# Kernel tuning notes

Hardware: AMD Instinct MI355X
Metric: run time of the kernel (lower is better)

## Reference

```python
import jax, jax.numpy as jnp
import numpy as np

H = 128        # hidden_dim
NP = 512       # program nodes
NV = 50000     # voxel nodes
E = 800000     # cross edges (16 per voxel)
TAU = 1.0
SLOPE = 0.01   # LeakyReLU default negative slope


def setup_inputs() -> dict:
    key = jax.random.key(0)
    ks = jax.random.split(key, 12)
    s = 1.0 / np.sqrt(H)
    x = jax.random.normal(ks[0], (NP, H), dtype=jnp.float32)
    v = jax.random.normal(ks[1], (NV, H), dtype=jnp.float32)
    row0 = jax.random.randint(ks[2], (E,), 0, NP, dtype=jnp.int32)
    row1 = (jnp.arange(E, dtype=jnp.int32) % NV)  # every voxel gets E/NV edges
    cross_edge_index = jnp.stack([row0, row1])    # [2, E]
    W_program = jax.random.normal(ks[3], (H, H), dtype=jnp.float32) * s
    b_program = jnp.zeros((H,), dtype=jnp.float32)
    W_voxel = jax.random.normal(ks[4], (H, H), dtype=jnp.float32) * s
    b_voxel = jnp.zeros((H,), dtype=jnp.float32)
    W_m1 = jax.random.normal(ks[5], (H, H), dtype=jnp.float32) * s
    b_m1 = jnp.zeros((H,), dtype=jnp.float32)
    W_m2 = jax.random.normal(ks[6], (H, 1), dtype=jnp.float32) * s
    b_m2 = jnp.zeros((1,), dtype=jnp.float32)
    theta = jax.random.normal(ks[7], (H, 1), dtype=jnp.float32) * s  # xavier-like
    u = jax.random.uniform(ks[8], (E,), dtype=jnp.float32)
    gumbel_u = jnp.clip(u, 1e-7, 1.0 - 1e-7)  # avoid log(0)
    return {"x": x, "v": v, "cross_edge_index": cross_edge_index,
            "W_program": W_program, "b_program": b_program,
            "W_voxel": W_voxel, "b_voxel": b_voxel,
            "W_m1": W_m1, "b_m1": b_m1, "W_m2": W_m2, "b_m2": b_m2,
            "theta": theta, "gumbel_u": gumbel_u}


def reference(x, v, cross_edge_index, W_program, b_program, W_voxel, b_voxel,
              W_m1, b_m1, W_m2, b_m2, theta, gumbel_u):
    src = cross_edge_index[0]
    dst = cross_edge_index[1]
    x_sel = x[src]                      # [E, H] gather
    v_sel = v[dst]                      # [E, H] gather
    # mask = sigmoid(MLP(v)) : Linear -> LeakyReLU -> Linear(H,1)
    a = v @ W_m1 + b_m1
    a = jnp.where(a >= 0, a, SLOPE * a)
    mask = jax.nn.sigmoid(a @ W_m2 + b_m2)                  # [NV, 1]
    # attention logits: theta^T * tanh(Wp x_sel + Wv v_sel), summed over H
    t = jnp.tanh(x_sel @ W_program + b_program + v_sel @ W_voxel + b_voxel)
    e = jnp.sum(t * theta[:, 0], axis=-1)                   # [E]
    # Gumbel softmax: global softmax over all edges (dim=0 in torch on 1-D e)
    g = -jnp.log(-jnp.log(gumbel_u))
    y = jax.nn.softmax((e + g) / TAU)                       # [E]
    # per-voxel hard argmax (scatter_max), straight-through estimator
    seg_max = jax.ops.segment_max(y, dst, num_segments=NV)  # [NV]
    is_max = y == seg_max[dst]
    cand = jnp.where(is_max, jnp.arange(E), E)
    argmax = jax.ops.segment_min(cand, dst, num_segments=NV)  # [NV], first max per voxel
    y_hard_1 = jnp.zeros(E + 1, y.dtype).at[argmax].set(1.0)[:E]  # overflow slot for empty segments
    y_hard = jax.lax.stop_gradient(y_hard_1 - y) + y
    # scatter-sum of soft-attended program features back to voxels
    summed = jax.ops.segment_sum(x_sel * y[:, None], dst, num_segments=NV)  # [NV, H]
    v_out = v + mask * summed
    return (v_out, mask, y[:, None], y_hard[:, None])
```

## Files before the change

kernel.cpp:

```cpp
#include <hip/hip_runtime.h>

#define H     128
#define NP    512
#define NVOX  50000
#define NEDGE 800000
#define EPV   16
#define SLOPE 0.01f
#define GR    16
#define NBLK  (NVOX / GR)
#define STRH  136
#define VSTR  132
#define C1    2.8853900817779268f
#define LOG2E 1.4426950408889634f
#define ABLK  3125

#define EXP2(x) __builtin_amdgcn_exp2f(x)
#define LOG2(x) __builtin_amdgcn_logf(x)
#define RCP(x)  __builtin_amdgcn_rcpf(x)

typedef _Float16 h16;
typedef __attribute__((ext_vector_type(4))) _Float16 h16x4;
typedef __attribute__((ext_vector_type(8))) _Float16 h16x8;
typedef __attribute__((ext_vector_type(4))) float    f32x4;

__global__ __launch_bounds__(256) void k_pre(const float* __restrict__ x,
                                             const float* __restrict__ Wp,
                                             const float* __restrict__ bp,
                                             const float* __restrict__ Wv,
                                             const float* __restrict__ Wm1,
                                             float* __restrict__ xpout,
                                             h16* __restrict__ WvThi,
                                             h16* __restrict__ WvTlo,
                                             h16* __restrict__ Wm1T) {
    __shared__ float part[H];
    int bid = blockIdx.x;
    int tid = threadIdx.x;
    if (bid < NP) {
        int row = bid;
        int col = tid & 127;
        int kh  = tid >> 7;
        int kbase = kh * 64;
        const float* xr = x + (size_t)row * H;
        float acc = 0.f;
#pragma unroll 8
        for (int k = 0; k < 64; ++k)
            acc = fmaf(xr[kbase + k], Wp[(size_t)(kbase + k) * H + col], acc);
        if (kh == 1) part[col] = acc;
        __syncthreads();
        if (kh == 0) xpout[(size_t)row * H + col] = (acc + part[col] + bp[col]) * C1;
    } else {
        int idx = (bid - NP) * 256 + tid;
        if (idx < 16384) {
            int k = idx >> 7, n = idx & 127;
            float w = Wv[idx];
            h16 hi = (h16)w;
            WvThi[n * H + k] = hi;
            WvTlo[n * H + k] = (h16)(w - (float)hi);
        } else {
            int j = idx - 16384;
            int k = j >> 7, n = j & 127;
            Wm1T[n * H + k] = (h16)Wm1[j];
        }
    }
}

__global__ __launch_bounds__(256) void k_main(
    const float* __restrict__ v,   const float* __restrict__ x,
    const float* __restrict__ bv,  const float* __restrict__ bm1,
    const float* __restrict__ Wm2, const float* __restrict__ bm2,
    const h16* __restrict__ WvThi, const h16* __restrict__ WvTlo,
    const h16* __restrict__ Wm1T,
    const float* __restrict__ xp,  const int* __restrict__ cei,
    const float* __restrict__ theta, const float* __restrict__ gum,
    float* __restrict__ mask_out, float* __restrict__ pout,
    float* __restrict__ sump,     float* __restrict__ partial)
{
    __shared__ __align__(16) char ldsbuf[2 * GR * STRH * 2];
    h16*   vh   = (h16*)ldsbuf;
    h16*   vl   = vh + GR * STRH;
    float* vt   = (float*)ldsbuf;
    float* scmb = (float*)ldsbuf;
    __shared__ float ptile[EPV * GR];
    __shared__ int   ceit[EPV * GR];
    __shared__ float gumt[EPV * GR];
    __shared__ int   amtile[GR];
    __shared__ float pmbuf[4][GR];
    __shared__ float psums[4];

    int tid  = threadIdx.x;
    int base = blockIdx.x * GR;

#pragma unroll
    for (int i = 0; i < 2; ++i) {
        int f  = i * 256 + tid;
        int r  = f >> 5, c4 = f & 31;
        float4 val = *(const float4*)&v[(size_t)(base + r) * H + c4 * 4];
        h16x4 hi, lo;
        hi.x = (h16)val.x; lo.x = (h16)(val.x - (float)hi.x);
        hi.y = (h16)val.y; lo.y = (h16)(val.y - (float)hi.y);
        hi.z = (h16)val.z; lo.z = (h16)(val.z - (float)hi.z);
        hi.w = (h16)val.w; lo.w = (h16)(val.w - (float)hi.w);
        *(h16x4*)&vh[r * STRH + c4 * 4] = hi;
        *(h16x4*)&vl[r * STRH + c4 * 4] = lo;
    }
    {
        int t = tid >> 4, c = tid & 15;
        int e = base + c + t * NVOX;
        ceit[tid] = cei[e];
        gumt[tid] = gum[e];
    }
    __syncthreads();

    int wave = tid >> 6, lane = tid & 63;
    int m16 = lane & 15, quad = lane >> 4;
    int cb = wave * 32;

    f32x4 aV[2], aM[2];
#pragma unroll
    for (int ct = 0; ct < 2; ++ct) { aV[ct] = (f32x4)0.f; aM[ct] = (f32x4)0.f; }

#pragma unroll
    for (int kc = 0; kc < 4; ++kc) {
        int kofs = kc * 32 + quad * 8;
        h16x8 ah = *(const h16x8*)&vh[m16 * STRH + kofs];
        h16x8 al = *(const h16x8*)&vl[m16 * STRH + kofs];
#pragma unroll
        for (int ct = 0; ct < 2; ++ct) {
            int n = cb + ct * 16 + m16;
            h16x8 bh = *(const h16x8*)&WvThi[n * H + kofs];
            h16x8 bl = *(const h16x8*)&WvTlo[n * H + kofs];
            h16x8 bm = *(const h16x8*)&Wm1T[n * H + kofs];
            aV[ct] = __builtin_amdgcn_mfma_f32_16x16x32_f16(ah, bh, aV[ct], 0, 0, 0);
            aV[ct] = __builtin_amdgcn_mfma_f32_16x16x32_f16(al, bh, aV[ct], 0, 0, 0);
            aV[ct] = __builtin_amdgcn_mfma_f32_16x16x32_f16(ah, bl, aV[ct], 0, 0, 0);
            aM[ct] = __builtin_amdgcn_mfma_f32_16x16x32_f16(ah, bm, aM[ct], 0, 0, 0);
        }
    }
    __syncthreads();

    float pml[4] = {0.f, 0.f, 0.f, 0.f};
#pragma unroll
    for (int ct = 0; ct < 2; ++ct) {
        int col = cb + ct * 16 + m16;
        float bvc = bv[col], bmc = bm1[col], w2c = Wm2[col];
#pragma unroll
        for (int reg = 0; reg < 4; ++reg) {
            int row = quad * 4 + reg;
            vt[row * VSTR + col] = (aV[ct][reg] + bvc) * C1;
            float m = aM[ct][reg] + bmc;
            m = (m >= 0.f) ? m : SLOPE * m;
            pml[reg] = fmaf(m, w2c, pml[reg]);
        }
    }
#pragma unroll
    for (int off = 8; off >= 1; off >>= 1)
#pragma unroll
        for (int reg = 0; reg < 4; ++reg)
            pml[reg] += __shfl_xor(pml[reg], off, 64);
    if (m16 == 0) {
#pragma unroll
        for (int reg = 0; reg < 4; ++reg)
            pmbuf[wave][quad * 4 + reg] = pml[reg];
    }
    __syncthreads();
    if (wave == 0 && lane < GR) {
        float s = pmbuf[0][lane] + pmbuf[1][lane] + pmbuf[2][lane]
                + pmbuf[3][lane] + bm2[0];
        mask_out[base + lane] = RCP(1.f + EXP2(-s * LOG2E));
    }

    int g = tid >> 3, lk = tid & 7;
    int vx = g & 15, half = g >> 4;
    float th2[16], thsum = 0.f;
#pragma unroll
    for (int i = 0; i < 4; ++i) {
        float4 t4 = *(const float4*)&theta[(lk + 8 * i) * 4];
        th2[i * 4 + 0] = -2.f * LOG2E * t4.x; th2[i * 4 + 1] = -2.f * LOG2E * t4.y;
        th2[i * 4 + 2] = -2.f * LOG2E * t4.z; th2[i * 4 + 3] = -2.f * LOG2E * t4.w;
        thsum += LOG2E * (t4.x + t4.y + t4.z + t4.w);
    }
    const float* vr = &vt[vx * VSTR];
    float4 b0 = *(const float4*)&vr[(lk +  0) * 4];
    float4 b1 = *(const float4*)&vr[(lk +  8) * 4];
    float4 b2 = *(const float4*)&vr[(lk + 16) * 4];
    float4 b3 = *(const float4*)&vr[(lk + 24) * 4];
    float wv8[8];
#pragma unroll
    for (int i = 0; i < 8; ++i)
        wv8[i] = -LOG2E * RCP(LOG2(gumt[(half * 8 + i) * GR + vx]));
    __syncthreads();

    float4 s0 = make_float4(0.f,0.f,0.f,0.f), s1 = s0, s2 = s0, s3 = s0;
#pragma unroll 2
    for (int i = 0; i < 8; ++i) {
        int t   = half * 8 + i;
        int src = ceit[t * GR + vx];
        const float4* xr = (const float4*)(xp + (size_t)src * H);
        const float4* xo = (const float4*)(x  + (size_t)src * H);
        float4 a0 = xr[lk], a1 = xr[lk + 8], a2 = xr[lk + 16], a3 = xr[lk + 24];
        float4 c0 = xo[lk], c1 = xo[lk + 8], c2 = xo[lk + 16], c3 = xo[lk + 24];
        float acc0 = thsum, acc1 = 0.f;
        acc0 = fmaf(th2[ 0], RCP(EXP2(a0.x + b0.x) + 1.f), acc0);
        acc1 = fmaf(th2[ 1], RCP(EXP2(a0.y + b0.y) + 1.f), acc1);
        acc0 = fmaf(th2[ 2], RCP(EXP2(a0.z + b0.z) + 1.f), acc0);
        acc1 = fmaf(th2[ 3], RCP(EXP2(a0.w + b0.w) + 1.f), acc1);
        acc0 = fmaf(th2[ 4], RCP(EXP2(a1.x + b1.x) + 1.f), acc0);
        acc1 = fmaf(th2[ 5], RCP(EXP2(a1.y + b1.y) + 1.f), acc1);
        acc0 = fmaf(th2[ 6], RCP(EXP2(a1.z + b1.z) + 1.f), acc0);
        acc1 = fmaf(th2[ 7], RCP(EXP2(a1.w + b1.w) + 1.f), acc1);
        acc0 = fmaf(th2[ 8], RCP(EXP2(a2.x + b2.x) + 1.f), acc0);
        acc1 = fmaf(th2[ 9], RCP(EXP2(a2.y + b2.y) + 1.f), acc1);
        acc0 = fmaf(th2[10], RCP(EXP2(a2.z + b2.z) + 1.f), acc0);
        acc1 = fmaf(th2[11], RCP(EXP2(a2.w + b2.w) + 1.f), acc1);
        acc0 = fmaf(th2[12], RCP(EXP2(a3.x + b3.x) + 1.f), acc0);
        acc1 = fmaf(th2[13], RCP(EXP2(a3.y + b3.y) + 1.f), acc1);
        acc0 = fmaf(th2[14], RCP(EXP2(a3.z + b3.z) + 1.f), acc0);
        acc1 = fmaf(th2[15], RCP(EXP2(a3.w + b3.w) + 1.f), acc1);
        float acc = acc0 + acc1;
        acc += __shfl_xor(acc, 4, 64);
        acc += __shfl_xor(acc, 2, 64);
        acc += __shfl_xor(acc, 1, 64);
        float p = EXP2(acc) * wv8[i];
        if (lk == 0) ptile[t * GR + vx] = p;
        s0.x = fmaf(p, c0.x, s0.x); s0.y = fmaf(p, c0.y, s0.y);
        s0.z = fmaf(p, c0.z, s0.z); s0.w = fmaf(p, c0.w, s0.w);
        s1.x = fmaf(p, c1.x, s1.x); s1.y = fmaf(p, c1.y, s1.y);
        s1.z = fmaf(p, c1.z, s1.z); s1.w = fmaf(p, c1.w, s1.w);
        s2.x = fmaf(p, c2.x, s2.x); s2.y = fmaf(p, c2.y, s2.y);
        s2.z = fmaf(p, c2.z, s2.z); s2.w = fmaf(p, c2.w, s2.w);
        s3.x = fmaf(p, c3.x, s3.x); s3.y = fmaf(p, c3.y, s3.y);
        s3.z = fmaf(p, c3.z, s3.z); s3.w = fmaf(p, c3.w, s3.w);
    }
    if (half == 1) {
        float* sc = scmb + vx * 128;
        *(float4*)&sc[(lk +  0) * 4] = s0;
        *(float4*)&sc[(lk +  8) * 4] = s1;
        *(float4*)&sc[(lk + 16) * 4] = s2;
        *(float4*)&sc[(lk + 24) * 4] = s3;
    }
    __syncthreads();
    if (tid < GR) {
        float mx = ptile[tid]; int a = 0;
#pragma unroll
        for (int t = 1; t < EPV; ++t) {
            float yv = ptile[t * GR + tid];
            if (yv > mx) { mx = yv; a = t; }
        }
        amtile[tid] = a;
    }
    if (half == 0) {
        const float* sc = scmb + vx * 128;
        float4 r0 = *(const float4*)&sc[(lk +  0) * 4];
        float4 r1 = *(const float4*)&sc[(lk +  8) * 4];
        float4 r2 = *(const float4*)&sc[(lk + 16) * 4];
        float4 r3 = *(const float4*)&sc[(lk + 24) * 4];
        float* sr = sump + (size_t)(base + vx) * H;
        *(float4*)&sr[(lk +  0) * 4] = make_float4(s0.x+r0.x, s0.y+r0.y, s0.z+r0.z, s0.w+r0.w);
        *(float4*)&sr[(lk +  8) * 4] = make_float4(s1.x+r1.x, s1.y+r1.y, s1.z+r1.z, s1.w+r1.w);
        *(float4*)&sr[(lk + 16) * 4] = make_float4(s2.x+r2.x, s2.y+r2.y, s2.z+r2.z, s2.w+r2.w);
        *(float4*)&sr[(lk + 24) * 4] = make_float4(s3.x+r3.x, s3.y+r3.y, s3.z+r3.z, s3.w+r3.w);
    }
    __syncthreads();
    float pv;
    {
        int t = tid >> 4, c = tid & 15;
        pv = ptile[tid];
        pout[base + c + t * NVOX] = (t == amtile[c]) ? -pv : pv;
    }
    float psum = pv;
#pragma unroll
    for (int off = 32; off >= 1; off >>= 1) psum += __shfl_xor(psum, off, 64);
    if (lane == 0) psums[wave] = psum;
    __syncthreads();
    if (tid == 0)
        partial[blockIdx.x] = psums[0] + psums[1] + psums[2] + psums[3];
}

__global__ __launch_bounds__(256) void k_reduce(const float* __restrict__ partial,
                                                float* __restrict__ invS) {
    __shared__ float wsum[4];
    int tid = threadIdx.x;
    float s = 0.f;
    for (int i = tid; i < NBLK; i += 256) s += partial[i];
#pragma unroll
    for (int off = 32; off >= 1; off >>= 1) s += __shfl_xor(s, off, 64);
    if ((tid & 63) == 0) wsum[tid >> 6] = s;
    __syncthreads();
    if (tid == 0) invS[0] = 1.f / (wsum[0] + wsum[1] + wsum[2] + wsum[3]);
}

__global__ __launch_bounds__(256) void k_out(const float* __restrict__ v,
                                             const float* __restrict__ maskp,
                                             const float* __restrict__ invSp,
                                             float* __restrict__ vout,
                                             float* __restrict__ ybuf,
                                             float* __restrict__ yhard) {
    float invS = invSp[0];
    int tid = threadIdx.x;
    int bid = blockIdx.x;
    if (bid < ABLK) {
#pragma unroll
        for (int r = 0; r < 2; ++r) {
            int i = (bid + r * ABLK) * 256 + tid;
            float4 sp = ((const float4*)vout)[i];
            float4 vv = ((const float4*)v)[i];
            float  m  = maskp[i >> 5] * invS;
            float4 o;
            o.x = fmaf(m, sp.x, vv.x); o.y = fmaf(m, sp.y, vv.y);
            o.z = fmaf(m, sp.z, vv.z); o.w = fmaf(m, sp.w, vv.w);
            ((float4*)vout)[i] = o;
        }
    } else {
        int e = (bid - ABLK) * 256 + tid;
        float pv = ybuf[e];
        ybuf[e]  = fabsf(pv) * invS;
        yhard[e] = (pv < 0.f) ? 1.f : 0.f;
    }
}

extern "C" void kernel_launch(void* const* d_in, const int* in_sizes, int n_in,
                              void* d_out, int out_size, void* d_ws, size_t ws_size,
                              hipStream_t stream) {
    (void)in_sizes; (void)n_in; (void)out_size; (void)ws_size;
    const float* x   = (const float*)d_in[0];
    const float* v   = (const float*)d_in[1];
    const int*   cei = (const int*)d_in[2];
    const float* Wp  = (const float*)d_in[3];
    const float* bp  = (const float*)d_in[4];
    const float* Wv  = (const float*)d_in[5];
    const float* bv  = (const float*)d_in[6];
    const float* Wm1 = (const float*)d_in[7];
    const float* bm1 = (const float*)d_in[8];
    const float* Wm2 = (const float*)d_in[9];
    const float* bm2 = (const float*)d_in[10];
    const float* th  = (const float*)d_in[11];
    const float* gum = (const float*)d_in[12];

    float* out   = (float*)d_out;
    float* vout  = out;
    float* maskp = out + (size_t)NVOX * H;
    float* ybuf  = maskp + NVOX;
    float* yhard = ybuf + NEDGE;
    float* xp    = yhard;
    h16*   WvThi = (h16*)(yhard + 65536);
    h16*   WvTlo = WvThi + 16384;
    h16*   Wm1T  = WvThi + 32768;
    float* partial = (float*)d_ws;
    float* invS    = (float*)d_ws + 4096;

    k_pre<<<NP + 128, 256, 0, stream>>>(x, Wp, bp, Wv, Wm1, xp, WvThi, WvTlo, Wm1T);
    k_main<<<NBLK, 256, 0, stream>>>(v, x, bv, bm1, Wm2, bm2, WvThi, WvTlo, Wm1T,
                                     xp, cei, th, gum, maskp, ybuf, vout, partial);
    k_reduce<<<1, 256, 0, stream>>>(partial, invS);
    k_out<<<2 * ABLK, 256, 0, stream>>>(v, maskp, invS, vout, ybuf, yhard);
}
```

Before: 197.4 us.

## Split fused voxel kernel into separate GEMM and edge-gather kernels

The single fused k_main kernel is split in two. k_gemm computes the voxel projection (split-fp16 MFMA) and the mask MLP for 32 voxels per block and writes the projected voxel features to a workspace buffer. k_edge then handles the per-edge tanh attention, Gumbel weighting, argmax and weighted scatter-sum with two voxels per wave. This is meant to give each phase its own occupancy and register profile in exchange for an extra NV×H fp32 write and read through global memory. The new path only runs when the workspace is large enough; otherwise the old fused path is used.

```diff
diff --git a/kernel.cpp b/kernel.cpp
--- a/kernel.cpp
+++ b/kernel.cpp
@@ -8,6 +8,10 @@
 #define SLOPE 0.01f
 #define GR    16
 #define NBLK  (NVOX / GR)
+#define GRG   32
+#define NBLKG ((NVOX + GRG - 1) / GRG)
+#define NEBLK (NVOX / 8)
+#define NPART (NEBLK * 4)
 #define STRH  136
 #define VSTR  132
 #define C1    2.8853900817779268f
@@ -61,6 +65,256 @@
             int k = j >> 7, n = j & 127;
             Wm1T[n * H + k] = (h16)Wm1[j];
         }
+    }
+}
+
+__global__ __launch_bounds__(256) void k_gemm(
+    const float* __restrict__ v,
+    const float* __restrict__ bv,  const float* __restrict__ bm1,
+    const float* __restrict__ Wm2, const float* __restrict__ bm2,
+    const h16* __restrict__ WvThi, const h16* __restrict__ WvTlo,
+    const h16* __restrict__ Wm1T,
+    float* __restrict__ vvg, float* __restrict__ mask_out)
+{
+    __shared__ __align__(16) h16 vh[GRG * STRH];
+    __shared__ __align__(16) h16 vl[GRG * STRH];
+    __shared__ float pmbuf[4][GRG];
+    int tid  = threadIdx.x;
+    int base = blockIdx.x * GRG;
+
+#pragma unroll
+    for (int i = 0; i < 4; ++i) {
+        int f  = i * 256 + tid;
+        int r  = f >> 5, c4 = f & 31;
+        int gr = base + r;
+        float4 val = (gr < NVOX) ? *(const float4*)&v[(size_t)gr * H + c4 * 4]
+                                 : make_float4(0.f, 0.f, 0.f, 0.f);
+        h16x4 hi, lo;
+        hi.x = (h16)val.x; lo.x = (h16)(val.x - (float)hi.x);
+        hi.y = (h16)val.y; lo.y = (h16)(val.y - (float)hi.y);
+        hi.z = (h16)val.z; lo.z = (h16)(val.z - (float)hi.z);
+        hi.w = (h16)val.w; lo.w = (h16)(val.w - (float)hi.w);
+        *(h16x4*)&vh[r * STRH + c4 * 4] = hi;
+        *(h16x4*)&vl[r * STRH + c4 * 4] = lo;
+    }
+    __syncthreads();
+
+    int wave = tid >> 6, lane = tid & 63;
+    int m16 = lane & 15, quad = lane >> 4;
+    int cb = wave * 32;
+
+    f32x4 aV[2][2], aM[2][2];
+#pragma unroll
+    for (int rt = 0; rt < 2; ++rt)
+#pragma unroll
+        for (int ct = 0; ct < 2; ++ct) { aV[rt][ct] = (f32x4)0.f; aM[rt][ct] = (f32x4)0.f; }
+
+#pragma unroll
+    for (int kc = 0; kc < 4; ++kc) {
+        int kofs = kc * 32 + quad * 8;
+        h16x8 ah[2], al[2];
+#pragma unroll
+        for (int rt = 0; rt < 2; ++rt) {
+            int row = rt * 16 + m16;
+            ah[rt] = *(const h16x8*)&vh[row * STRH + kofs];
+            al[rt] = *(const h16x8*)&vl[row * STRH + kofs];
+        }
+#pragma unroll
+        for (int ct = 0; ct < 2; ++ct) {
+            int n = cb + ct * 16 + m16;
+            h16x8 bh = *(const h16x8*)&WvThi[n * H + kofs];
+            h16x8 bl = *(const h16x8*)&WvTlo[n * H + kofs];
+            h16x8 bm = *(const h16x8*)&Wm1T[n * H + kofs];
+#pragma unroll
+            for (int rt = 0; rt < 2; ++rt) {
+                aV[rt][ct] = __builtin_amdgcn_mfma_f32_16x16x32_f16(ah[rt], bh, aV[rt][ct], 0, 0, 0);
+                aV[rt][ct] = __builtin_amdgcn_mfma_f32_16x16x32_f16(al[rt], bh, aV[rt][ct], 0, 0, 0);
+                aV[rt][ct] = __builtin_amdgcn_mfma_f32_16x16x32_f16(ah[rt], bl, aV[rt][ct], 0, 0, 0);
+                aM[rt][ct] = __builtin_amdgcn_mfma_f32_16x16x32_f16(ah[rt], bm, aM[rt][ct], 0, 0, 0);
+            }
+        }
+    }
+
+    float pml[2][4];
+#pragma unroll
+    for (int rt = 0; rt < 2; ++rt)
+#pragma unroll
+        for (int reg = 0; reg < 4; ++reg) pml[rt][reg] = 0.f;
+#pragma unroll
+    for (int ct = 0; ct < 2; ++ct) {
+        int col = cb + ct * 16 + m16;
+        float bvc = bv[col], bmc = bm1[col], w2c = Wm2[col];
+#pragma unroll
+        for (int rt = 0; rt < 2; ++rt)
+#pragma unroll
+            for (int reg = 0; reg < 4; ++reg) {
+                int grow = base + rt * 16 + quad * 4 + reg;
+                if (grow < NVOX)
+                    vvg[(size_t)grow * H + col] = (aV[rt][ct][reg] + bvc) * C1;
+                float m = aM[rt][ct][reg] + bmc;
+                m = (m >= 0.f) ? m : SLOPE * m;
+                pml[rt][reg] = fmaf(m, w2c, pml[rt][reg]);
+            }
+    }
+#pragma unroll
+    for (int off = 8; off >= 1; off >>= 1)
+#pragma unroll
+        for (int rt = 0; rt < 2; ++rt)
+#pragma unroll
+            for (int reg = 0; reg < 4; ++reg)
+                pml[rt][reg] += __shfl_xor(pml[rt][reg], off, 64);
+    if (m16 == 0) {
+#pragma unroll
+        for (int rt = 0; rt < 2; ++rt)
+#pragma unroll
+            for (int reg = 0; reg < 4; ++reg)
+                pmbuf[wave][rt * 16 + quad * 4 + reg] = pml[rt][reg];
+    }
+    __syncthreads();
+    if (wave == 0 && lane < GRG) {
+        int gr = base + lane;
+        if (gr < NVOX) {
+            float s = pmbuf[0][lane] + pmbuf[1][lane] + pmbuf[2][lane]
+                    + pmbuf[3][lane] + bm2[0];
+            mask_out[gr] = RCP(1.f + EXP2(-s * LOG2E));
+        }
+    }
+}
+
+__global__ __launch_bounds__(256) void k_edge(
+    const float* __restrict__ x,   const float* __restrict__ xp,
+    const float* __restrict__ vvg, const int* __restrict__ cei,
+    const float* __restrict__ theta, const float* __restrict__ gum,
+    float* __restrict__ pout, float* __restrict__ sump,
+    float* __restrict__ partial)
+{
+    int tid  = threadIdx.x;
+    int w    = tid >> 6, lane = tid & 63;
+    int gw   = lane >> 4, lk = lane & 15;
+    int half = gw >> 1;
+    int vox  = blockIdx.x * 8 + w * 2 + (gw & 1);
+
+    const float4* th4 = (const float4*)theta;
+    float4 t0 = th4[lk], t1 = th4[lk + 16];
+    float th2[8];
+    th2[0] = -2.f * LOG2E * t0.x; th2[1] = -2.f * LOG2E * t0.y;
+    th2[2] = -2.f * LOG2E * t0.z; th2[3] = -2.f * LOG2E * t0.w;
+    th2[4] = -2.f * LOG2E * t1.x; th2[5] = -2.f * LOG2E * t1.y;
+    th2[6] = -2.f * LOG2E * t1.z; th2[7] = -2.f * LOG2E * t1.w;
+    float thsum = LOG2E * (t0.x + t0.y + t0.z + t0.w + t1.x + t1.y + t1.z + t1.w);
+
+    const float4* vv4 = (const float4*)(vvg + (size_t)vox * H);
+    float4 B0 = vv4[lk], B1 = vv4[lk + 16];
+
+    float wv8[8];
+#pragma unroll
+    for (int i = 0; i < 8; ++i)
+        wv8[i] = -LOG2E * RCP(LOG2(gum[vox + (half * 8 + i) * NVOX]));
+
+    float4 s0 = make_float4(0.f, 0.f, 0.f, 0.f), s1 = s0;
+    float pregs[8];
+    float pmax = -1.f, psg = 0.f;
+    int   pidx = 0;
+#pragma unroll 2
+    for (int i = 0; i < 8; ++i) {
+        int t   = half * 8 + i;
+        int src = cei[vox + t * NVOX];
+        const float4* xr = (const float4*)(xp + (size_t)src * H);
+        const float4* xo = (const float4*)(x  + (size_t)src * H);
+        float4 a0 = xr[lk], a1 = xr[lk + 16];
+        float4 c0 = xo[lk], c1 = xo[lk + 16];
+        float acc0 = thsum, acc1 = 0.f;
+        acc0 = fmaf(th2[0], RCP(EXP2(a0.x + B0.x) + 1.f), acc0);
+        acc1 = fmaf(th2[1], RCP(EXP2(a0.y + B0.y) + 1.f), acc1);
+        acc0 = fmaf(th2[2], RCP(EXP2(a0.z + B0.z) + 1.f), acc0);
+        acc1 = fmaf(th2[3], RCP(EXP2(a0.w + B0.w) + 1.f), acc1);
+        acc0 = fmaf(th2[4], RCP(EXP2(a1.x + B1.x) + 1.f), acc0);
+        acc1 = fmaf(th2[5], RCP(EXP2(a1.y + B1.y) + 1.f), acc1);
+        acc0 = fmaf(th2[6], RCP(EXP2(a1.z + B1.z) + 1.f), acc0);
+        acc1 = fmaf(th2[7], RCP(EXP2(a1.w + B1.w) + 1.f), acc1);
+        float acc = acc0 + acc1;
+        acc += __shfl_xor(acc, 1, 64);
+        acc += __shfl_xor(acc, 2, 64);
+        acc += __shfl_xor(acc, 4, 64);
+        acc += __shfl_xor(acc, 8, 64);
+        float p = EXP2(acc) * wv8[i];
+        pregs[i] = p;
+        if (p > pmax) { pmax = p; pidx = t; }
+        psg += p;
+        s0.x = fmaf(p, c0.x, s0.x); s0.y = fmaf(p, c0.y, s0.y);
+        s0.z = fmaf(p, c0.z, s0.z); s0.w = fmaf(p, c0.w, s0.w);
+        s1.x = fmaf(p, c1.x, s1.x); s1.y = fmaf(p, c1.y, s1.y);
+        s1.z = fmaf(p, c1.z, s1.z); s1.w = fmaf(p, c1.w, s1.w);
+    }
+    s0.x += __shfl_xor(s0.x, 32, 64); s0.y += __shfl_xor(s0.y, 32, 64);
+    s0.z += __shfl_xor(s0.z, 32, 64); s0.w += __shfl_xor(s0.w, 32, 64);
+    s1.x += __shfl_xor(s1.x, 32, 64); s1.y += __shfl_xor(s1.y, 32, 64);
+    s1.z += __shfl_xor(s1.z, 32, 64); s1.w += __shfl_xor(s1.w, 32, 64);
+    float pmo = __shfl_xor(pmax, 32, 64);
+    int   pio = __shfl_xor(pidx, 32, 64);
+    float pmA = half ? pmo : pmax;  int piA = half ? pio : pidx;
+    float pmB = half ? pmax : pmo;  int piB = half ? pidx : pio;
+    int am = (pmB > pmA) ? piB : piA;
+
+    if (half == 0) {
+        float4* sp = (float4*)(sump + (size_t)vox * H);
+        sp[lk]      = s0;
+        sp[lk + 16] = s1;
+    }
+    if (lk == 0) {
+#pragma unroll
+        for (int i = 0; i < 8; ++i) {
+            int t = half * 8 + i;
+            float val = pregs[i];
+            pout[vox + t * NVOX] = (t == am) ? -val : val;
+        }
+    }
+    float ps_full = psg + __shfl_xor(psg, 32, 64);
+    float contrib = (lk == 0 && half == 0) ? ps_full : 0.f;
+    contrib += __shfl_xor(contrib, 16, 64);
+    contrib += __shfl_xor(contrib, 32, 64);
+    if (lane == 0) partial[blockIdx.x * 4 + w] = contrib;
+}
+
+__global__ __launch_bounds__(256) void k_reduce(const float* __restrict__ partial,
+                                                int n, float* __restrict__ invS) {
+    __shared__ float wsum[4];
+    int tid = threadIdx.x;
+    float s = 0.f;
+    for (int i = tid; i < n; i += 256) s += partial[i];
+#pragma unroll
+    for (int off = 32; off >= 1; off >>= 1) s += __shfl_xor(s, off, 64);
+    if ((tid & 63) == 0) wsum[tid >> 6] = s;
+    __syncthreads();
+    if (tid == 0) invS[0] = 1.f / (wsum[0] + wsum[1] + wsum[2] + wsum[3]);
+}
+
+__global__ __launch_bounds__(256) void k_out(const float* __restrict__ v,
+                                             const float* __restrict__ maskp,
+                                             const float* __restrict__ invSp,
+                                             float* __restrict__ vout,
+                                             float* __restrict__ ybuf,
+                                             float* __restrict__ yhard) {
+    float invS = invSp[0];
+    int tid = threadIdx.x;
+    int bid = blockIdx.x;
+    if (bid < ABLK) {
+#pragma unroll
+        for (int r = 0; r < 2; ++r) {
+            int i = (bid + r * ABLK) * 256 + tid;
+            float4 sp = ((const float4*)vout)[i];
+            float4 vv = ((const float4*)v)[i];
+            float  m  = maskp[i >> 5] * invS;
+            float4 o;
+            o.x = fmaf(m, sp.x, vv.x); o.y = fmaf(m, sp.y, vv.y);
+            o.z = fmaf(m, sp.z, vv.z); o.w = fmaf(m, sp.w, vv.w);
+            ((float4*)vout)[i] = o;
+        }
+    } else {
+        int e = (bid - ABLK) * 256 + tid;
+        float pv = ybuf[e];
+        ybuf[e]  = fabsf(pv) * invS;
+        yhard[e] = (pv < 0.f) ? 1.f : 0.f;
     }
 }
 
@@ -276,52 +530,10 @@
         partial[blockIdx.x] = psums[0] + psums[1] + psums[2] + psums[3];
 }
 
-__global__ __launch_bounds__(256) void k_reduce(const float* __restrict__ partial,
-                                                float* __restrict__ invS) {
-    __shared__ float wsum[4];
-    int tid = threadIdx.x;
-    float s = 0.f;
-    for (int i = tid; i < NBLK; i += 256) s += partial[i];
-#pragma unroll
-    for (int off = 32; off >= 1; off >>= 1) s += __shfl_xor(s, off, 64);
-    if ((tid & 63) == 0) wsum[tid >> 6] = s;
-    __syncthreads();
-    if (tid == 0) invS[0] = 1.f / (wsum[0] + wsum[1] + wsum[2] + wsum[3]);
-}
-
-__global__ __launch_bounds__(256) void k_out(const float* __restrict__ v,
-                                             const float* __restrict__ maskp,
-                                             const float* __restrict__ invSp,
-                                             float* __restrict__ vout,
-                                             float* __restrict__ ybuf,
-                                             float* __restrict__ yhard) {
-    float invS = invSp[0];
-    int tid = threadIdx.x;
-    int bid = blockIdx.x;
-    if (bid < ABLK) {
-#pragma unroll
-        for (int r = 0; r < 2; ++r) {
-            int i = (bid + r * ABLK) * 256 + tid;
-            float4 sp = ((const float4*)vout)[i];
-            float4 vv = ((const float4*)v)[i];
-            float  m  = maskp[i >> 5] * invS;
-            float4 o;
-            o.x = fmaf(m, sp.x, vv.x); o.y = fmaf(m, sp.y, vv.y);
-            o.z = fmaf(m, sp.z, vv.z); o.w = fmaf(m, sp.w, vv.w);
-            ((float4*)vout)[i] = o;
-        }
-    } else {
-        int e = (bid - ABLK) * 256 + tid;
-        float pv = ybuf[e];
-        ybuf[e]  = fabsf(pv) * invS;
-        yhard[e] = (pv < 0.f) ? 1.f : 0.f;
-    }
-}
-
 extern "C" void kernel_launch(void* const* d_in, const int* in_sizes, int n_in,
                               void* d_out, int out_size, void* d_ws, size_t ws_size,
                               hipStream_t stream) {
-    (void)in_sizes; (void)n_in; (void)out_size; (void)ws_size;
+    (void)in_sizes; (void)n_in; (void)out_size;
     const float* x   = (const float*)d_in[0];
     const float* v   = (const float*)d_in[1];
     const int*   cei = (const int*)d_in[2];
@@ -345,12 +557,25 @@
     h16*   WvThi = (h16*)(yhard + 65536);
     h16*   WvTlo = WvThi + 16384;
     h16*   Wm1T  = WvThi + 32768;
-    float* partial = (float*)d_ws;
-    float* invS    = (float*)d_ws + 4096;
-
-    k_pre<<<NP + 128, 256, 0, stream>>>(x, Wp, bp, Wv, Wm1, xp, WvThi, WvTlo, Wm1T);
-    k_main<<<NBLK, 256, 0, stream>>>(v, x, bv, bm1, Wm2, bm2, WvThi, WvTlo, Wm1T,
-                                     xp, cei, th, gum, maskp, ybuf, vout, partial);
-    k_reduce<<<1, 256, 0, stream>>>(partial, invS);
-    k_out<<<2 * ABLK, 256, 0, stream>>>(v, maskp, invS, vout, ybuf, yhard);
-}
+
+    size_t need = ((size_t)NVOX * H + 40000) * sizeof(float);
+    if (ws_size >= need) {
+        float* vvg     = (float*)d_ws;
+        float* partial = vvg + (size_t)NVOX * H;
+        float* invS    = partial + 32768;
+        k_pre<<<NP + 128, 256, 0, stream>>>(x, Wp, bp, Wv, Wm1, xp, WvThi, WvTlo, Wm1T);
+        k_gemm<<<NBLKG, 256, 0, stream>>>(v, bv, bm1, Wm2, bm2, WvThi, WvTlo, Wm1T,
+                                          vvg, maskp);
+        k_edge<<<NEBLK, 256, 0, stream>>>(x, xp, vvg, cei, th, gum, ybuf, vout, partial);
+        k_reduce<<<1, 256, 0, stream>>>(partial, NPART, invS);
+        k_out<<<2 * ABLK, 256, 0, stream>>>(v, maskp, invS, vout, ybuf, yhard);
+    } else {
+        float* partial = (float*)d_ws;
+        float* invS    = (float*)d_ws + 4096;
+        k_pre<<<NP + 128, 256, 0, stream>>>(x, Wp, bp, Wv, Wm1, xp, WvThi, WvTlo, Wm1T);
+        k_main<<<NBLK, 256, 0, stream>>>(v, x, bv, bm1, Wm2, bm2, WvThi, WvTlo, Wm1T,
+                                         xp, cei, th, gum, maskp, ybuf, vout, partial);
+        k_reduce<<<1, 256, 0, stream>>>(partial, NBLK, invS);
+        k_out<<<2 * ABLK, 256, 0, stream>>>(v, maskp, invS, vout, ybuf, yhard);
+    }
+}
```

New measurement: 223.3 us. 13.2% more time.
